# Kernel optimization log

Hardware: AMD Instinct MI355X
Metric: run time of the kernel (lower is better)

## Reference

```python
import jax, jax.numpy as jnp
import numpy as np

N = 50000      # nodes per node type
E = 800000     # edges per meta-step (avg degree 16)
DIN = 16       # input feature dim (all node types)
DMSG = 16      # dim_message per meta-step
F = 16         # edge feature dim
DOUT = 32      # dim_out of final linear


def setup_inputs() -> dict:
    key = jax.random.key(0)
    ks = jax.random.split(key, 17)
    s = 0.1  # param scale
    return {
        "x_indivi": jax.random.normal(ks[0], (N, DIN), jnp.float32),
        "x_src_a": jax.random.normal(ks[1], (N, DIN), jnp.float32),
        "x_src_b": jax.random.normal(ks[2], (N, DIN), jnp.float32),
        "edge_index_a": jax.random.randint(ks[3], (2, E), 0, N),
        "edge_index_b": jax.random.randint(ks[4], (2, E), 0, N),
        "edge_attr_a": jax.random.normal(ks[5], (E, F), jnp.float32),
        "edge_attr_b": jax.random.normal(ks[6], (E, F), jnp.float32),
        # message_function of NNConv: Linear(F, DIN*DMSG), stored as [F, DIN, DMSG]
        "w_msg_a": jax.random.normal(ks[7], (F, DIN, DMSG), jnp.float32) * s,
        "b_msg_a": jax.random.normal(ks[8], (DIN, DMSG), jnp.float32) * s,
        "root_a": jax.random.normal(ks[9], (DIN, DMSG), jnp.float32) * s,
        "bias_a": jax.random.normal(ks[10], (DMSG,), jnp.float32) * s,
        "w_msg_b": jax.random.normal(ks[11], (F, DIN, DMSG), jnp.float32) * s,
        "b_msg_b": jax.random.normal(ks[12], (DIN, DMSG), jnp.float32) * s,
        "root_b": jax.random.normal(ks[13], (DIN, DMSG), jnp.float32) * s,
        "bias_b": jax.random.normal(ks[14], (DMSG,), jnp.float32) * s,
        # final linear: Linear(2*DMSG, DOUT), stored as [2*DMSG, DOUT]
        "w_lin": jax.random.normal(ks[15], (2 * DMSG, DOUT), jnp.float32) * s,
        "b_lin": jax.random.normal(ks[16], (DOUT,), jnp.float32) * s,
    }


def _nnconv(x_src, x_dst, edge_index, edge_attr, w_msg, b_msg, root, bias):
    """PyG NNConv with sum aggregation.
    W_e = edge_attr @ w_msg + b_msg  (per-edge [DIN, DMSG] weight matrix)
    msg_e = x_src[src_e] @ W_e ; out = segment_sum(msg) + x_dst @ root + bias
    """
    src, dst = edge_index[0], edge_index[1]
    xj = x_src[src]  # [E, DIN] gather
    # fused per-edge bmm: einsum contracts without keeping W_e longer than needed
    msg = jnp.einsum('ef,fio,ei->eo', edge_attr, w_msg, xj) + xj @ b_msg  # [E, DMSG]
    agg = jax.ops.segment_sum(msg, dst, num_segments=x_dst.shape[0])  # scatter-add
    return agg + x_dst @ root + bias


def reference(x_indivi, x_src_a, x_src_b, edge_index_a, edge_index_b,
              edge_attr_a, edge_attr_b,
              w_msg_a, b_msg_a, root_a, bias_a,
              w_msg_b, b_msg_b, root_b, bias_b,
              w_lin, b_lin):
    msg_a = jax.nn.sigmoid(_nnconv(x_src_a, x_indivi, edge_index_a, edge_attr_a,
                                   w_msg_a, b_msg_a, root_a, bias_a))
    msg_b = jax.nn.sigmoid(_nnconv(x_src_b, x_indivi, edge_index_b, edge_attr_b,
                                   w_msg_b, b_msg_b, root_b, bias_b))
    msg_cat = jnp.concatenate([msg_a, msg_b], axis=1)  # [N, 2*DMSG]
    return jax.nn.sigmoid(msg_cat @ w_lin + b_lin)     # [N, DOUT]
```

## Files before the change

kernel.cpp:

```cpp
#include <hip/hip_runtime.h>
#include <hip/hip_bf16.h>
#include <stdint.h>


#define NN 50000
#define EE 800000

typedef __attribute__((ext_vector_type(8))) short short8;
typedef __attribute__((ext_vector_type(4))) float f32x4;

union U8 { short8 v; unsigned int u[4]; };

__device__ __forceinline__ unsigned short f2bf_rne(float f) {
    union { float fl; unsigned int i; } v; v.fl = f;
    unsigned int x = v.i;
    x += 0x7FFFu + ((x >> 16) & 1u);
    return (unsigned short)(x >> 16);
}

__device__ __forceinline__ unsigned int pack2bf(float a, float b) {
    __hip_bfloat162 h = __float22bfloat162_rn(float2{a, b});
    union { __hip_bfloat162 h2; unsigned int u; } c; c.h2 = h;
    return c.u;
}

__global__ void prep_w(const float* __restrict__ w_msg_a, const float* __restrict__ b_msg_a,
                       unsigned short* __restrict__ wf_a,
                       const float* __restrict__ w_msg_b, const float* __restrict__ b_msg_b,
                       unsigned short* __restrict__ wf_b) {
    const float* w_msg = blockIdx.x ? w_msg_b : w_msg_a;
    const float* b_msg = blockIdx.x ? b_msg_b : b_msg_a;
    unsigned short* wfrag = blockIdx.x ? wf_b : wf_a;
    for (int idx = threadIdx.x; idx < 9 * 64 * 8; idx += 256) {
        int j = idx & 7;
        int lane = (idx >> 3) & 63;
        int t = idx >> 9;
        int k = 32 * t + (lane >> 4) * 8 + j;
        int n = lane & 15;
        int f = k >> 4, i = k & 15;
        float v = (f < 16) ? w_msg[f * 256 + i * 16 + n]
                           : (f == 16 ? b_msg[i * 16 + n] : 0.f);
        wfrag[idx] = f2bf_rne(v);
    }
}

__global__ __launch_bounds__(256) void edge_mfma(
    const int* __restrict__ ei_a, const float* __restrict__ ea_a,
    const float* __restrict__ x_a, const unsigned short* __restrict__ wf_a,
    float* __restrict__ agg_a,
    const int* __restrict__ ei_b, const float* __restrict__ ea_b,
    const float* __restrict__ x_b, const unsigned short* __restrict__ wf_b,
    float* __restrict__ agg_b)
{
    int ms = blockIdx.x & 1;
    const int* __restrict__ eidx  = ms ? ei_b : ei_a;
    const float* __restrict__ attr = ms ? ea_b : ea_a;
    const float* __restrict__ x    = ms ? x_b : x_a;
    const unsigned short* __restrict__ wfrag = ms ? wf_b : wf_a;
    float* __restrict__ agg = ms ? agg_b : agg_a;

    int lane = threadIdx.x & 63;
    int m = lane & 15, quad = lane >> 4;
    int q2 = quad >> 1, qb = quad & 1;
    int wave = ((blockIdx.x >> 1) * 256 + (int)threadIdx.x) >> 6;
    int nwaves = (gridDim.x >> 1) * 4;

    short8 bfr[9];
    #pragma unroll
    for (int t = 0; t < 9; ++t)
        bfr[t] = ((const short8*)wfrag)[t * 64 + lane];

    for (int g = wave; g < EE / 16; g += nwaves) {
        int ebase = g * 16;
        int src = eidx[ebase + m];
        int dstr[4];
        #pragma unroll
        for (int r = 0; r < 4; ++r)
            dstr[r] = eidx[EE + ebase + quad * 4 + r];

        const float4* xr = (const float4*)(x + (size_t)src * 16);
        float4 x0 = xr[qb * 2];
        float4 x1 = xr[qb * 2 + 1];
        float xh[8] = {x0.x, x0.y, x0.z, x0.w, x1.x, x1.y, x1.z, x1.w};

        const float* ar = attr + (size_t)(ebase + m) * 16;
        float ah[8];
        #pragma unroll
        for (int t = 0; t < 8; ++t) ah[t] = ar[2 * t + q2];

        f32x4 acc = {0.f, 0.f, 0.f, 0.f};
        #pragma unroll
        for (int t = 0; t < 8; ++t) {
            U8 a;
            #pragma unroll
            for (int jj = 0; jj < 4; ++jj)
                a.u[jj] = pack2bf(ah[t] * xh[2 * jj], ah[t] * xh[2 * jj + 1]);
            acc = __builtin_amdgcn_mfma_f32_16x16x32_bf16(a.v, bfr[t], acc, 0, 0, 0);
        }
        U8 a8;
        #pragma unroll
        for (int jj = 0; jj < 4; ++jj)
            a8.u[jj] = (q2 == 0) ? pack2bf(xh[2 * jj], xh[2 * jj + 1]) : 0u;
        acc = __builtin_amdgcn_mfma_f32_16x16x32_bf16(a8.v, bfr[8], acc, 0, 0, 0);

        #pragma unroll
        for (int r = 0; r < 4; ++r)
            atomicAdd(&agg[dstr[r] * 16 + m], acc[r]);
    }
}

__global__ __launch_bounds__(256) void finalize(
    const float* __restrict__ xind,
    const float* __restrict__ agg_a, const float* __restrict__ agg_b,
    const float* __restrict__ root_a, const float* __restrict__ bias_a,
    const float* __restrict__ root_b, const float* __restrict__ bias_b,
    const float* __restrict__ w_lin, const float* __restrict__ b_lin,
    float* __restrict__ out)
{
    int tid = threadIdx.x;
    int n = blockIdx.x * 8 + (tid >> 5);
    if (n >= NN) return;
    int d = tid & 31;
    int lane = tid & 63;
    int gb32 = lane & ~31;

    float xv = xind[n * 16 + (d & 15)];

    int j = d & 15;
    const float* root = (d < 16) ? root_a : root_b;
    const float* bias = (d < 16) ? bias_a : bias_b;
    const float* agg  = (d < 16) ? agg_a  : agg_b;

    float acc = agg[n * 16 + j] + bias[j];
    #pragma unroll
    for (int i = 0; i < 16; ++i) {
        float xiv = __shfl(xv, gb32 + i);
        acc += xiv * root[i * 16 + j];
    }
    float h = 1.f / (1.f + __expf(-acc));

    float acc2 = b_lin[d];
    #pragma unroll
    for (int jj = 0; jj < 32; ++jj) {
        float hj = __shfl(h, gb32 + jj);
        acc2 += hj * w_lin[jj * 32 + d];
    }
    out[(size_t)n * 32 + d] = 1.f / (1.f + __expf(-acc2));
}

extern "C" void kernel_launch(void* const* d_in, const int* in_sizes, int n_in,
                              void* d_out, int out_size, void* d_ws, size_t ws_size,
                              hipStream_t stream) {
    (void)in_sizes; (void)n_in; (void)out_size; (void)ws_size;
    const float* x_indivi = (const float*)d_in[0];
    const float* x_src_a  = (const float*)d_in[1];
    const float* x_src_b  = (const float*)d_in[2];
    const int*   ei_a     = (const int*)d_in[3];
    const int*   ei_b     = (const int*)d_in[4];
    const float* ea_a     = (const float*)d_in[5];
    const float* ea_b     = (const float*)d_in[6];
    const float* w_msg_a  = (const float*)d_in[7];
    const float* b_msg_a  = (const float*)d_in[8];
    const float* root_a   = (const float*)d_in[9];
    const float* bias_a   = (const float*)d_in[10];
    const float* w_msg_b  = (const float*)d_in[11];
    const float* b_msg_b  = (const float*)d_in[12];
    const float* root_b   = (const float*)d_in[13];
    const float* bias_b   = (const float*)d_in[14];
    const float* w_lin    = (const float*)d_in[15];
    const float* b_lin    = (const float*)d_in[16];
    float* out = (float*)d_out;

    char* ws = (char*)d_ws;
    size_t off = 0;
    unsigned short* wf_a = (unsigned short*)(ws + off); off += 9 * 64 * 8 * 2;
    unsigned short* wf_b = (unsigned short*)(ws + off); off += 9 * 64 * 8 * 2;
    float* agg_a = (float*)(ws + off); off += (size_t)NN * 16 * 4;
    float* agg_b = (float*)(ws + off); off += (size_t)NN * 16 * 4;

    hipMemsetAsync(agg_a, 0, (size_t)NN * 16 * 4 * 2, stream);
    prep_w<<<2, 256, 0, stream>>>(w_msg_a, b_msg_a, wf_a, w_msg_b, b_msg_b, wf_b);

    edge_mfma<<<2048, 256, 0, stream>>>(ei_a, ea_a, x_src_a, wf_a, agg_a,
                                        ei_b, ea_b, x_src_b, wf_b, agg_b);

    finalize<<<(NN + 7) / 8, 256, 0, stream>>>(
        x_indivi, agg_a, agg_b, root_a, bias_a, root_b, bias_b, w_lin, b_lin, out);
}
```

Before: 292.5 us.

## Replace atomic scatter-add with destination-sorted buckets and per-bucket partial sums

Result: slower. 607.3 us (+107.6%).

```diff
diff --git a/kernel.cpp b/kernel.cpp
--- a/kernel.cpp
+++ b/kernel.cpp
@@ -5,6 +5,8 @@
 
 #define NN 50000
 #define EE 800000
+#define SLOT 1600000
+#define BN   100000
 
 typedef __attribute__((ext_vector_type(8))) short short8;
 typedef __attribute__((ext_vector_type(4))) float f32x4;
@@ -44,20 +46,93 @@
     }
 }
 
-__global__ __launch_bounds__(256) void edge_mfma(
-    const int* __restrict__ ei_a, const float* __restrict__ ea_a,
-    const float* __restrict__ x_a, const unsigned short* __restrict__ wf_a,
-    float* __restrict__ agg_a,
-    const int* __restrict__ ei_b, const float* __restrict__ ea_b,
-    const float* __restrict__ x_b, const unsigned short* __restrict__ wf_b,
-    float* __restrict__ agg_b)
+__global__ __launch_bounds__(256) void hist(const int* __restrict__ ei_a,
+                                            const int* __restrict__ ei_b,
+                                            unsigned int* __restrict__ cnt) {
+    int idx = blockIdx.x * 256 + threadIdx.x;
+    int ms = idx >= EE;
+    int el = idx - ms * EE;
+    const int* ei = ms ? ei_b : ei_a;
+    atomicAdd(&cnt[ms * NN + ei[EE + el]], 1u);
+}
+
+__global__ __launch_bounds__(1024) void scan_fill(const unsigned int* __restrict__ cnt,
+                                                  unsigned int* __restrict__ cursor,
+                                                  unsigned int* __restrict__ bstart,
+                                                  unsigned int* __restrict__ binfo) {
+    int ms = blockIdx.x;
+    const unsigned int* c = cnt + ms * NN;
+    unsigned int* cur = cursor + ms * NN;
+    unsigned int* bs = bstart + ms * (NN + 1);
+    unsigned int* bi = binfo + ms * BN;
+    int t = threadIdx.x;
+    const int C = 49;
+    int s0 = t * C, s1 = s0 + C;
+    if (s1 > NN) s1 = NN;
+    if (s0 > NN) s0 = NN;
+
+    unsigned int acc = 0;
+    for (int n = s0; n < s1; ++n)
+        acc += max(1u, (c[n] + 15u) >> 4);
+
+    __shared__ unsigned int sA[1024], sB[1024];
+    sA[t] = acc;
+    __syncthreads();
+    unsigned int* src = sA; unsigned int* dst = sB;
+    for (int d = 1; d < 1024; d <<= 1) {
+        unsigned int v = src[t] + ((t >= d) ? src[t - d] : 0u);
+        dst[t] = v;
+        __syncthreads();
+        unsigned int* tmp = src; src = dst; dst = tmp;
+    }
+    unsigned int b = (t == 0) ? 0u : src[t - 1];
+
+    for (int n = s0; n < s1; ++n) {
+        unsigned int bc = max(1u, (c[n] + 15u) >> 4);
+        bs[n] = b;
+        cur[n] = b * 16u;
+        for (unsigned int k = 0; k < bc; ++k)
+            bi[b + k] = ((unsigned int)n << 16) | k;
+        b += bc;
+    }
+    if (s1 == NN && s0 < NN) bs[NN] = b;
+}
+
+__global__ __launch_bounds__(256) void scatter(const int* __restrict__ ei_a,
+                                               const int* __restrict__ ei_b,
+                                               unsigned int* __restrict__ cursor,
+                                               int* __restrict__ srcid,
+                                               int* __restrict__ eid) {
+    int idx = blockIdx.x * 256 + threadIdx.x;
+    int ms = idx >= EE;
+    int el = idx - ms * EE;
+    const int* ei = ms ? ei_b : ei_a;
+    int d = ei[EE + el];
+    unsigned int pos = atomicAdd(&cursor[ms * NN + d], 1u);
+    srcid[ms * SLOT + pos] = ei[el];
+    eid[ms * SLOT + pos]   = el;
+}
+
+__global__ __launch_bounds__(256) void edge_mfma_s(
+    const float* __restrict__ ea_a, const float* __restrict__ x_a,
+    const unsigned short* __restrict__ wf_a,
+    const float* __restrict__ ea_b, const float* __restrict__ x_b,
+    const unsigned short* __restrict__ wf_b,
+    const unsigned int* __restrict__ cnt, const unsigned int* __restrict__ bstart,
+    const unsigned int* __restrict__ binfo,
+    const int* __restrict__ srcid, const int* __restrict__ eid,
+    float* __restrict__ bpart)
 {
     int ms = blockIdx.x & 1;
-    const int* __restrict__ eidx  = ms ? ei_b : ei_a;
-    const float* __restrict__ attr = ms ? ea_b : ea_a;
-    const float* __restrict__ x    = ms ? x_b : x_a;
-    const unsigned short* __restrict__ wfrag = ms ? wf_b : wf_a;
-    float* __restrict__ agg = ms ? agg_b : agg_a;
+    const float* attr = ms ? ea_b : ea_a;
+    const float* x    = ms ? x_b : x_a;
+    const unsigned short* wfrag = ms ? wf_b : wf_a;
+    const unsigned int* c  = cnt + ms * NN;
+    const unsigned int* bi = binfo + ms * BN;
+    const int* sid  = srcid + ms * SLOT;
+    const int* eidm = eid + ms * SLOT;
+    float* bp = bpart + (size_t)ms * BN * 16;
+    int nb = (int)bstart[ms * (NN + 1) + NN];
 
     int lane = threadIdx.x & 63;
     int m = lane & 15, quad = lane >> 4;
@@ -70,23 +145,32 @@
     for (int t = 0; t < 9; ++t)
         bfr[t] = ((const short8*)wfrag)[t * 64 + lane];
 
-    for (int g = wave; g < EE / 16; g += nwaves) {
-        int ebase = g * 16;
-        int src = eidx[ebase + m];
-        int dstr[4];
-        #pragma unroll
-        for (int r = 0; r < 4; ++r)
-            dstr[r] = eidx[EE + ebase + quad * 4 + r];
-
-        const float4* xr = (const float4*)(x + (size_t)src * 16);
-        float4 x0 = xr[qb * 2];
-        float4 x1 = xr[qb * 2 + 1];
+    for (int g = wave; g < nb; g += nwaves) {
+        unsigned int info = bi[g];
+        int n = (int)(info >> 16);
+        int k = (int)(info & 0xFFFFu);
+        int vc = (int)c[n] - k * 16;
+        bool ok = m < vc;
+        int slot = g * 16 + m;
+        int ev = eidm[slot];
+        int sv = sid[slot];
+        int ea = ok ? ev : 0;
+        int sa = ok ? sv : 0;
+
+        const f32x4* xr = (const f32x4*)(x + (size_t)sa * 16);
+        f32x4 x0 = xr[qb * 2];
+        f32x4 x1 = xr[qb * 2 + 1];
         float xh[8] = {x0.x, x0.y, x0.z, x0.w, x1.x, x1.y, x1.z, x1.w};
-
-        const float* ar = attr + (size_t)(ebase + m) * 16;
+        #pragma unroll
+        for (int j = 0; j < 8; ++j) xh[j] = ok ? xh[j] : 0.f;
+
+        const float* ar = attr + (size_t)ea * 16;
         float ah[8];
         #pragma unroll
-        for (int t = 0; t < 8; ++t) ah[t] = ar[2 * t + q2];
+        for (int t = 0; t < 8; ++t) {
+            float av = ar[2 * t + q2];
+            ah[t] = ok ? av : 0.f;
+        }
 
         f32x4 acc = {0.f, 0.f, 0.f, 0.f};
         #pragma unroll
@@ -103,15 +187,16 @@
             a8.u[jj] = (q2 == 0) ? pack2bf(xh[2 * jj], xh[2 * jj + 1]) : 0u;
         acc = __builtin_amdgcn_mfma_f32_16x16x32_bf16(a8.v, bfr[8], acc, 0, 0, 0);
 
-        #pragma unroll
-        for (int r = 0; r < 4; ++r)
-            atomicAdd(&agg[dstr[r] * 16 + m], acc[r]);
+        float s = acc[0] + acc[1] + acc[2] + acc[3];
+        s += __shfl_xor(s, 16);
+        s += __shfl_xor(s, 32);
+        if (lane < 16) bp[(size_t)g * 16 + lane] = s;
     }
 }
 
 __global__ __launch_bounds__(256) void finalize(
     const float* __restrict__ xind,
-    const float* __restrict__ agg_a, const float* __restrict__ agg_b,
+    const unsigned int* __restrict__ bstart, const float* __restrict__ bpart,
     const float* __restrict__ root_a, const float* __restrict__ bias_a,
     const float* __restrict__ root_b, const float* __restrict__ bias_b,
     const float* __restrict__ w_lin, const float* __restrict__ b_lin,
@@ -129,9 +214,13 @@
     int j = d & 15;
     const float* root = (d < 16) ? root_a : root_b;
     const float* bias = (d < 16) ? bias_a : bias_b;
-    const float* agg  = (d < 16) ? agg_a  : agg_b;
-
-    float acc = agg[n * 16 + j] + bias[j];
+    const unsigned int* bs = bstart + ((d < 16) ? 0 : (NN + 1));
+    const float* bp = bpart + ((d < 16) ? 0 : (size_t)BN * 16);
+
+    float acc = bias[j];
+    unsigned int b0 = bs[n], b1 = bs[n + 1];
+    for (unsigned int b = b0; b < b1; ++b)
+        acc += bp[(size_t)b * 16 + j];
     #pragma unroll
     for (int i = 0; i < 16; ++i) {
         float xiv = __shfl(xv, gb32 + i);
@@ -147,6 +236,8 @@
     }
     out[(size_t)n * 32 + d] = 1.f / (1.f + __expf(-acc2));
 }
+
+static inline size_t align512(size_t x) { return (x + 511) & ~(size_t)511; }
 
 extern "C" void kernel_launch(void* const* d_in, const int* in_sizes, int n_in,
                               void* d_out, int out_size, void* d_ws, size_t ws_size,
@@ -173,17 +264,23 @@
 
     char* ws = (char*)d_ws;
     size_t off = 0;
-    unsigned short* wf_a = (unsigned short*)(ws + off); off += 9 * 64 * 8 * 2;
-    unsigned short* wf_b = (unsigned short*)(ws + off); off += 9 * 64 * 8 * 2;
-    float* agg_a = (float*)(ws + off); off += (size_t)NN * 16 * 4;
-    float* agg_b = (float*)(ws + off); off += (size_t)NN * 16 * 4;
-
-    hipMemsetAsync(agg_a, 0, (size_t)NN * 16 * 4 * 2, stream);
+    unsigned short* wf_a = (unsigned short*)(ws + off); off = align512(off + 9 * 64 * 8 * 2);
+    unsigned short* wf_b = (unsigned short*)(ws + off); off = align512(off + 9 * 64 * 8 * 2);
+    unsigned int* cnt    = (unsigned int*)(ws + off);   off = align512(off + 2 * NN * 4);
+    unsigned int* cursor = (unsigned int*)(ws + off);   off = align512(off + 2 * NN * 4);
+    unsigned int* bstart = (unsigned int*)(ws + off);   off = align512(off + 2 * (NN + 1) * 4);
+    unsigned int* binfo  = (unsigned int*)(ws + off);   off = align512(off + 2 * (size_t)BN * 4);
+    int* srcid           = (int*)(ws + off);            off = align512(off + 2 * (size_t)SLOT * 4);
+    int* eid             = (int*)(ws + off);            off = align512(off + 2 * (size_t)SLOT * 4);
+    float* bpart         = (float*)(ws + off);          off = align512(off + 2 * (size_t)BN * 16 * 4);
+
+    (void)hipMemsetAsync(cnt, 0, 2 * NN * 4, stream);
     prep_w<<<2, 256, 0, stream>>>(w_msg_a, b_msg_a, wf_a, w_msg_b, b_msg_b, wf_b);
-
-    edge_mfma<<<2048, 256, 0, stream>>>(ei_a, ea_a, x_src_a, wf_a, agg_a,
-                                        ei_b, ea_b, x_src_b, wf_b, agg_b);
-
+    hist<<<(2 * EE) / 256, 256, 0, stream>>>(ei_a, ei_b, cnt);
+    scan_fill<<<2, 1024, 0, stream>>>(cnt, cursor, bstart, binfo);
+    scatter<<<(2 * EE) / 256, 256, 0, stream>>>(ei_a, ei_b, cursor, srcid, eid);
+    edge_mfma_s<<<4096, 256, 0, stream>>>(ea_a, x_src_a, wf_a, ea_b, x_src_b, wf_b,
+                                          cnt, bstart, binfo, srcid, eid, bpart);
     finalize<<<(NN + 7) / 8, 256, 0, stream>>>(
-        x_indivi, agg_a, agg_b, root_a, bias_a, root_b, bias_b, w_lin, b_lin, out);
-}
+        x_indivi, bstart, bpart, root_a, bias_a, root_b, bias_b, w_lin, b_lin, out);
+}
```
